# Kernel tuning notes

Measured on AMD Instinct MI355X. Metric: run time of the kernel, lower is better.

## Reference

```python
import jax, jax.numpy as jnp
import numpy as np

N, E = 50000, 800000
IN_DIM, HID, H1, H2, NCLS = 512, 64, 4, 1, 40
NEG_SLOPE = 0.2


def gat_conv(x, src, dst, W, att_src, att_dst, b, heads, ch):
    # x: [N, F_in]; W: [F_in, heads*ch]; att_*: [heads, ch]; b: [heads*ch]
    n = x.shape[0]
    h = (x @ W).reshape(n, heads, ch)                      # [N,H,C]
    a_s = jnp.einsum('nhc,hc->nh', h, att_src)             # [N,H]
    a_d = jnp.einsum('nhc,hc->nh', h, att_dst)             # [N,H]
    e = jax.nn.leaky_relu(a_s[src] + a_d[dst], NEG_SLOPE)  # [E,H]
    # segment softmax over incoming edges of each destination node
    m = jax.ops.segment_max(e, dst, num_segments=n)        # [N,H]
    ex = jnp.exp(e - m[dst])
    s = jax.ops.segment_sum(ex, dst, num_segments=n)       # [N,H]
    alpha = ex / (s[dst] + 1e-16)                          # [E,H]
    out = jax.ops.segment_sum(alpha[:, :, None] * h[src], dst, num_segments=n)
    return out.reshape(n, heads * ch) + b


def setup_inputs() -> dict:
    key = jax.random.key(0)
    ks = jax.random.split(key, 10)
    glorot = lambda k, shp: jax.random.normal(k, shp, jnp.float32) * jnp.sqrt(2.0 / (shp[0] + shp[-1]))
    return {
        'x': jax.random.normal(ks[0], (N, IN_DIM), jnp.float32),
        'edge_index': jax.random.randint(ks[1], (2, E), 0, N, jnp.int64),
        'W1': glorot(ks[2], (IN_DIM, H1 * HID)),
        'att_src1': glorot(ks[3], (H1, HID)),
        'att_dst1': glorot(ks[4], (H1, HID)),
        'b1': jnp.zeros((H1 * HID,), jnp.float32),
        'W2': glorot(ks[5], (H1 * HID, H2 * NCLS)),
        'att_src2': glorot(ks[6], (H2, NCLS)),
        'att_dst2': glorot(ks[7], (H2, NCLS)),
        'b2': jnp.zeros((H2 * NCLS,), jnp.float32),
    }


def reference(x, edge_index, W1, att_src1, att_dst1, b1, W2, att_src2, att_dst2, b2):
    n = x.shape[0]
    loops = jnp.arange(n, dtype=edge_index.dtype)
    src = jnp.concatenate([edge_index[0], loops])  # add self loops (PyG default)
    dst = jnp.concatenate([edge_index[1], loops])
    # dropout layers are identity in eval mode
    h = gat_conv(x, src, dst, W1, att_src1, att_dst1, b1, H1, HID)
    h = jax.nn.elu(h)
    out = gat_conv(h, src, dst, W2, att_src2, att_dst2, b2, H2, NCLS)
    return jax.nn.log_softmax(out, axis=1)
```

## Files before the change

### kernel.cpp

```cpp
#include <hip/hip_runtime.h>
#include <math.h>
#include <stdint.h>


typedef short bf16x8 __attribute__((ext_vector_type(8)));
typedef float f32x4  __attribute__((ext_vector_type(4)));

static __device__ __forceinline__ float leaky(float x){ return x > 0.f ? x : 0.2f*x; }
static __device__ __forceinline__ unsigned short f2bf(float f){
  uint32_t u = __float_as_uint(f);
  uint32_t r = u + 0x7fffu + ((u >> 16) & 1u);
  return (unsigned short)(r >> 16);
}
static __device__ __forceinline__ float bf2f(unsigned short u){
  return __uint_as_float(((uint32_t)u) << 16);
}

__global__ void k_cvt_w(const float* __restrict__ W, unsigned short* __restrict__ wt,
                        int* __restrict__ deg, int n){
  int i = blockIdx.x*blockDim.x + threadIdx.x;
  if (i < n) deg[i] = 0;
  if (i >= 256*64) return;
  int col = i & 255, kg = i >> 8;
  int kt = kg >> 2, kq = kg & 3;
  unsigned short* dst = wt + ((size_t)kt*1024 + kq*256 + col)*8;
  bf16x8 p;
  #pragma unroll
  for (int j=0;j<8;j++) p[j] = (short)f2bf(W[(size_t)(kg*8+j)*256 + col]);
  *(bf16x8*)dst = p;
}

__global__ void k_count(const int* __restrict__ ei, int E, int n, int* __restrict__ deg){
  int i = blockIdx.x*blockDim.x + threadIdx.x;
  int tot = E + n;
  if (i >= tot) return;
  int dst = (i < E) ? ei[E + i] : (i - E);
  atomicAdd(&deg[dst], 1);
}

__global__ __launch_bounds__(256) void k_scan_a(const int* __restrict__ deg,
    int* __restrict__ rowstart, int* __restrict__ bsum, int n){
  __shared__ int sm[256];
  int b = blockIdx.x, t = threadIdx.x;
  int i = b*256 + t;
  int v = (i < n) ? deg[i] : 0;
  sm[t] = v;
  __syncthreads();
  for (int off=1; off<256; off<<=1){
    int u = (t >= off) ? sm[t-off] : 0;
    __syncthreads();
    sm[t] += u;
    __syncthreads();
  }
  if (i < n) rowstart[i+1] = sm[t];
  if (t == 255) bsum[b] = sm[255];
}
__global__ __launch_bounds__(256) void k_scan_b(int* __restrict__ bsum, int nb){
  __shared__ int sm[256];
  int t = threadIdx.x;
  int v = (t < nb) ? bsum[t] : 0;
  sm[t] = v;
  __syncthreads();
  for (int off=1; off<256; off<<=1){
    int u = (t >= off) ? sm[t-off] : 0;
    __syncthreads();
    sm[t] += u;
    __syncthreads();
  }
  if (t < nb) bsum[t] = sm[t] - v;
}
__global__ __launch_bounds__(256) void k_scan_c(int* __restrict__ rowstart,
    const int* __restrict__ bsum, int* __restrict__ cur, int n){
  int b = blockIdx.x, t = threadIdx.x;
  int i = b*256 + t;
  if (i < n){ rowstart[i+1] += bsum[b]; cur[i] = 0; }
  if (i == 0) rowstart[0] = 0;
}

__global__ __launch_bounds__(256, 6) void k_gemm1_mfma(const float* __restrict__ X,
                                                    const unsigned short* __restrict__ WT,
                                                    const float* __restrict__ SW,
                                                    const float* __restrict__ DW,
                                                    unsigned short* __restrict__ Cb,
                                                    float* __restrict__ as1,
                                                    float* __restrict__ ad1, int M){
  __shared__ __align__(16) unsigned short lA[2][2048];
  __shared__ __align__(16) unsigned short lB[2][4096];
  const int t = threadIdx.x;
  const int lane = t & 63, w = t >> 6;
  const int wx = w & 1, wy = w >> 1;
  const int row0 = blockIdx.x * 64, col0 = blockIdx.y * 128;

  f32x4 acc[2][4];
  #pragma unroll
  for (int i=0;i<2;i++)
    #pragma unroll
    for (int j=0;j<4;j++)
      #pragma unroll
      for (int r=0;r<4;r++) acc[i][j][r] = 0.f;

  const int rA = w*16 + (lane & 15);
  const int kA = lane >> 4;
  const float* xA = X + (size_t)min(row0 + rA, M-1)*512 + kA*8;
  const int aChunk = kA*64 + rA;

  const int c0 = t, c1 = t + 256;
  const unsigned short* bB0 = WT + ((size_t)(c0>>7)*256 + col0 + (c0&127))*8;
  const unsigned short* bB1 = WT + ((size_t)(c1>>7)*256 + col0 + (c1&127))*8;

  const int fkq = lane >> 4, li = lane & 15;

#define ISSUE_B(NXT, KT) do{ \
  __builtin_amdgcn_global_load_lds((const __attribute__((address_space(1))) void*)(bB0 + (size_t)(KT)*8192), \
      (__attribute__((address_space(3))) void*)&lB[NXT][c0*8], 16, 0, 0); \
  __builtin_amdgcn_global_load_lds((const __attribute__((address_space(1))) void*)(bB1 + (size_t)(KT)*8192), \
      (__attribute__((address_space(3))) void*)&lB[NXT][c1*8], 16, 0, 0); }while(0)

#define CVT_WRITE(NXT, S0,S1) do{ \
  bf16x8 p0; \
  p0[0]=(short)f2bf(S0.x); p0[1]=(short)f2bf(S0.y); p0[2]=(short)f2bf(S0.z); p0[3]=(short)f2bf(S0.w); \
  p0[4]=(short)f2bf(S1.x); p0[5]=(short)f2bf(S1.y); p0[6]=(short)f2bf(S1.z); p0[7]=(short)f2bf(S1.w); \
  *(bf16x8*)&lA[NXT][aChunk*8] = p0; }while(0)

#define STEP(T, CUR) do{ \
  float4 n0, n1; \
  if ((T) < 15){ \
    n0 = *(const float4*)(xA + ((T)+1)*32); \
    n1 = *(const float4*)(xA + ((T)+1)*32 + 4); \
    ISSUE_B((CUR)^1, (T)+1); \
  } \
  bf16x8 af[2], bfr[4]; \
  _Pragma("unroll") \
  for (int i=0;i<2;i++) \
    af[i]  = *(const bf16x8*)&lA[CUR][(fkq*64 + wx*32 + i*16 + li)*8]; \
  _Pragma("unroll") \
  for (int j=0;j<4;j++) \
    bfr[j] = *(const bf16x8*)&lB[CUR][(fkq*128 + wy*64 + j*16 + li)*8]; \
  _Pragma("unroll") \
  for (int i=0;i<2;i++) \
    _Pragma("unroll") \
    for (int j=0;j<4;j++) \
      acc[i][j] = __builtin_amdgcn_mfma_f32_16x16x32_bf16(af[i], bfr[j], acc[i][j], 0, 0, 0); \
  if ((T) < 15){ \
    CVT_WRITE((CUR)^1, n0, n1); \
    __syncthreads(); \
  } \
}while(0)

  {
    float4 a0 = *(const float4*)(xA);
    float4 a1 = *(const float4*)(xA + 4);
    ISSUE_B(0, 0);
    CVT_WRITE(0, a0, a1);
    __syncthreads();
  }

  #pragma unroll
  for (int tt = 0; tt < 8; ++tt){
    STEP(2*tt,   (0));
    STEP(2*tt+1, (1));
  }

#undef STEP
#undef CVT_WRITE
#undef ISSUE_B

  #pragma unroll
  for (int i=0;i<2;i++){
    #pragma unroll
    for (int r=0;r<4;r++){
      int row = row0 + wx*32 + i*16 + fkq*4 + r;
      if (row < M){
        #pragma unroll
        for (int j=0;j<4;j++)
          Cb[(size_t)row*256 + col0 + wy*64 + j*16 + li] = f2bf(acc[i][j][r]);
      }
    }
  }

  const int hw = (int)blockIdx.y*2 + wy;
  float sv[4], dv[4];
  #pragma unroll
  for (int j=0;j<4;j++){
    sv[j] = SW[hw*64 + j*16 + li];
    dv[j] = DW[hw*64 + j*16 + li];
  }
  #pragma unroll
  for (int i=0;i<2;i++){
    #pragma unroll
    for (int r=0;r<4;r++){
      float ps = acc[i][0][r]*sv[0] + acc[i][1][r]*sv[1] + acc[i][2][r]*sv[2] + acc[i][3][r]*sv[3];
      float pd = acc[i][0][r]*dv[0] + acc[i][1][r]*dv[1] + acc[i][2][r]*dv[2] + acc[i][3][r]*dv[3];
      #pragma unroll
      for (int o=1;o<16;o<<=1){ ps += __shfl_xor(ps,o); pd += __shfl_xor(pd,o); }
      int row = row0 + wx*32 + i*16 + fkq*4 + r;
      if (li == 0 && row < M){
        as1[row*4 + hw] = ps;
        ad1[row*4 + hw] = pd;
      }
    }
  }
}

__global__ void k_fill(const int* __restrict__ ei, int E, int n,
                       const int* __restrict__ rowstart, int* __restrict__ cur,
                       int* __restrict__ csr,
                       const float* __restrict__ as1, const float* __restrict__ ad1,
                       float* __restrict__ exbuf){
  int i = blockIdx.x*blockDim.x + threadIdx.x;
  int tot = E + n;
  if (i >= tot) return;
  int src, dst;
  if (i < E){ src = ei[i]; dst = ei[E+i]; } else { src = i - E; dst = src; }
  int pos = atomicAdd(&cur[dst], 1);
  int slot = rowstart[dst] + pos;
  csr[slot] = src;
  float4 a = *(const float4*)(as1 + (size_t)src*4);
  float4 d = *(const float4*)(ad1 + (size_t)dst*4);
  float4 ex;
  ex.x = __expf(fminf(leaky(a.x + d.x), 80.f));
  ex.y = __expf(fminf(leaky(a.y + d.y), 80.f));
  ex.z = __expf(fminf(leaky(a.z + d.z), 80.f));
  ex.w = __expf(fminf(leaky(a.w + d.w), 80.f));
  *(float4*)(exbuf + (size_t)slot*4) = ex;
}

__global__ __launch_bounds__(256) void k_agg1(const unsigned short* __restrict__ h1b,
    const float* __restrict__ exbuf,
    const int* __restrict__ rowstart, const int* __restrict__ csr,
    const float* __restrict__ b1, unsigned short* __restrict__ hactb, int n){
  int lane = threadIdx.x & 63;
  int node = blockIdx.x*4 + (threadIdx.x >> 6);
  if (node >= n) return;
  int lo = __builtin_amdgcn_readfirstlane(rowstart[node]);
  int hi = __builtin_amdgcn_readfirstlane(rowstart[node+1]);
  int h = lane >> 4;
  const float* exb = exbuf + h;
  float ax=0.f, ay=0.f, az=0.f, aw=0.f, psum=0.f;
  int e = lo;
  for (; e + 7 < hi; e += 8){
    int s0 = csr[e],   s1 = csr[e+1], s2 = csr[e+2], s3 = csr[e+3];
    int s4 = csr[e+4], s5 = csr[e+5], s6 = csr[e+6], s7 = csr[e+7];
    float e0 = exb[(size_t)e*4],     e1 = exb[(size_t)(e+1)*4],
          e2 = exb[(size_t)(e+2)*4], e3 = exb[(size_t)(e+3)*4],
          e4 = exb[(size_t)(e+4)*4], e5 = exb[(size_t)(e+5)*4],
          e6 = exb[(size_t)(e+6)*4], e7 = exb[(size_t)(e+7)*4];
    ushort4 u0 = *(const ushort4*)(h1b + (size_t)s0*256 + lane*4);
    ushort4 u1 = *(const ushort4*)(h1b + (size_t)s1*256 + lane*4);
    ushort4 u2 = *(const ushort4*)(h1b + (size_t)s2*256 + lane*4);
    ushort4 u3 = *(const ushort4*)(h1b + (size_t)s3*256 + lane*4);
    ushort4 u4 = *(const ushort4*)(h1b + (size_t)s4*256 + lane*4);
    ushort4 u5 = *(const ushort4*)(h1b + (size_t)s5*256 + lane*4);
    ushort4 u6 = *(const ushort4*)(h1b + (size_t)s6*256 + lane*4);
    ushort4 u7 = *(const ushort4*)(h1b + (size_t)s7*256 + lane*4);
    ax += e0*bf2f(u0.x) + e1*bf2f(u1.x) + e2*bf2f(u2.x) + e3*bf2f(u3.x)
        + e4*bf2f(u4.x) + e5*bf2f(u5.x) + e6*bf2f(u6.x) + e7*bf2f(u7.x);
    ay += e0*bf2f(u0.y) + e1*bf2f(u1.y) + e2*bf2f(u2.y) + e3*bf2f(u3.y)
        + e4*bf2f(u4.y) + e5*bf2f(u5.y) + e6*bf2f(u6.y) + e7*bf2f(u7.y);
    az += e0*bf2f(u0.z) + e1*bf2f(u1.z) + e2*bf2f(u2.z) + e3*bf2f(u3.z)
        + e4*bf2f(u4.z) + e5*bf2f(u5.z) + e6*bf2f(u6.z) + e7*bf2f(u7.z);
    aw += e0*bf2f(u0.w) + e1*bf2f(u1.w) + e2*bf2f(u2.w) + e3*bf2f(u3.w)
        + e4*bf2f(u4.w) + e5*bf2f(u5.w) + e6*bf2f(u6.w) + e7*bf2f(u7.w);
    psum += (e0+e1+e2+e3) + (e4+e5+e6+e7);
  }
  for (; e < hi; ++e){
    int s0 = csr[e];
    float e0 = exb[(size_t)e*4];
    ushort4 u0 = *(const ushort4*)(h1b + (size_t)s0*256 + lane*4);
    ax += e0*bf2f(u0.x); ay += e0*bf2f(u0.y); az += e0*bf2f(u0.z); aw += e0*bf2f(u0.w);
    psum += e0;
  }
  float inv = 1.f/(psum + 1e-16f);
  float4 bv = *(const float4*)(b1 + lane*4);
  float o0 = ax*inv + bv.x, o1 = ay*inv + bv.y, o2 = az*inv + bv.z, o3 = aw*inv + bv.w;
  ushort4 r;
  r.x = f2bf(o0 > 0.f ? o0 : expm1f(o0));
  r.y = f2bf(o1 > 0.f ? o1 : expm1f(o1));
  r.z = f2bf(o2 > 0.f ? o2 : expm1f(o2));
  r.w = f2bf(o3 > 0.f ? o3 : expm1f(o3));
  *(ushort4*)(hactb + (size_t)node*256 + lane*4) = r;
}

__global__ __launch_bounds__(256) void k_gemm2(const unsigned short* __restrict__ A,
    const float* __restrict__ B, const float* __restrict__ sw, const float* __restrict__ dw,
    unsigned short* __restrict__ Cb, float* __restrict__ as2, float* __restrict__ ad2, int M){
  __shared__ float Xl[32][129];
  __shared__ float Wl[128*40];
  __shared__ float Sps[32][8], Spd[32][8];
  int t = threadIdx.x;
  int row0 = blockIdx.x*32;
  int r = t & 31, g = t >> 5;
  float acc[5] = {0,0,0,0,0};
  for (int kt=0; kt<256; kt+=128){
    for (int i=t; i<1280; i+=256)
      *(float4*)&Wl[i*4] = *(const float4*)(B + kt*40 + i*4);
    for (int i=t; i<512; i+=256){
      int rr = i >> 4, k8 = i & 15;
      int grow = row0 + rr; if (grow >= M) grow = M-1;
      uint4 v = *(const uint4*)(A + (size_t)grow*256 + kt + k8*8);
      float* xp = &Xl[rr][k8*8];
      xp[0] = __uint_as_float(v.x << 16); xp[1] = __uint_as_float(v.x & 0xffff0000u);
      xp[2] = __uint_as_float(v.y << 16); xp[3] = __uint_as_float(v.y & 0xffff0000u);
      xp[4] = __uint_as_float(v.z << 16); xp[5] = __uint_as_float(v.z & 0xffff0000u);
      xp[6] = __uint_as_float(v.w << 16); xp[7] = __uint_as_float(v.w & 0xffff0000u);
    }
    __syncthreads();
    #pragma unroll 4
    for (int k=0;k<128;++k){
      float a = Xl[r][k];
      const float* wp = &Wl[k*40 + g*5];
      #pragma unroll
      for (int j=0;j<5;++j) acc[j] += a * wp[j];
    }
    __syncthreads();
  }
  int grow = row0 + r;
  float ps = 0.f, pd = 0.f;
  #pragma unroll
  for (int j=0;j<5;++j){
    ps += acc[j] * sw[g*5+j];
    pd += acc[j] * dw[g*5+j];
  }
  Sps[r][g] = ps; Spd[r][g] = pd;
  if (grow < M){
    #pragma unroll
    for (int j=0;j<5;++j) Cb[(size_t)grow*40 + g*5 + j] = f2bf(acc[j]);
  }
  __syncthreads();
  if (t < 32){
    float a = 0.f, b = 0.f;
    #pragma unroll
    for (int g2=0; g2<8; ++g2){ a += Sps[t][g2]; b += Spd[t][g2]; }
    int rw = row0 + t;
    if (rw < M){ as2[rw] = a; ad2[rw] = b; }
  }
}

__global__ __launch_bounds__(256) void k_pre2(const float* __restrict__ as2,
    const float* __restrict__ ad2, const int* __restrict__ rowstart,
    const int* __restrict__ csr, float* __restrict__ ex2, int n){
  int lane = threadIdx.x & 63;
  int node = blockIdx.x*4 + (threadIdx.x >> 6);
  if (node >= n) return;
  int lo = rowstart[node], hi = rowstart[node+1];
  float adn = ad2[node];
  for (int e = lo + lane; e < hi; e += 64)
    ex2[e] = __expf(fminf(leaky(as2[csr[e]] + adn), 80.f));
}

__global__ __launch_bounds__(256) void k_agg2(const unsigned short* __restrict__ h2b,
    const float* __restrict__ ex2,
    const int* __restrict__ rowstart, const int* __restrict__ csr,
    const float* __restrict__ b2, float* __restrict__ out, int n){
  int lane = threadIdx.x & 63;
  int node = blockIdx.x*4 + (threadIdx.x >> 6);
  if (node >= n) return;
  int lo = __builtin_amdgcn_readfirstlane(rowstart[node]);
  int hi = __builtin_amdgcn_readfirstlane(rowstart[node+1]);
  bool act = lane < 40;
  float acc = 0.f, psum = 0.f;
  int e = lo;
  for (; e + 7 < hi; e += 8){
    int s0 = csr[e],   s1 = csr[e+1], s2 = csr[e+2], s3 = csr[e+3];
    int s4 = csr[e+4], s5 = csr[e+5], s6 = csr[e+6], s7 = csr[e+7];
    float e0 = ex2[e],   e1 = ex2[e+1], e2 = ex2[e+2], e3 = ex2[e+3];
    float e4 = ex2[e+4], e5 = ex2[e+5], e6 = ex2[e+6], e7 = ex2[e+7];
    float h0 = act ? bf2f(h2b[(size_t)s0*40 + lane]) : 0.f;
    float h1 = act ? bf2f(h2b[(size_t)s1*40 + lane]) : 0.f;
    float h2 = act ? bf2f(h2b[(size_t)s2*40 + lane]) : 0.f;
    float h3 = act ? bf2f(h2b[(size_t)s3*40 + lane]) : 0.f;
    float h4 = act ? bf2f(h2b[(size_t)s4*40 + lane]) : 0.f;
    float h5 = act ? bf2f(h2b[(size_t)s5*40 + lane]) : 0.f;
    float h6 = act ? bf2f(h2b[(size_t)s6*40 + lane]) : 0.f;
    float h7 = act ? bf2f(h2b[(size_t)s7*40 + lane]) : 0.f;
    acc += e0*h0 + e1*h1 + e2*h2 + e3*h3 + e4*h4 + e5*h5 + e6*h6 + e7*h7;
    psum += (e0+e1+e2+e3) + (e4+e5+e6+e7);
  }
  for (; e < hi; ++e){
    int s0 = csr[e]; float e0 = ex2[e];
    acc += e0 * (act ? bf2f(h2b[(size_t)s0*40 + lane]) : 0.f);
    psum += e0;
  }
  float ov = acc/(psum + 1e-16f) + (act ? b2[lane] : 0.f);
  float v = act ? ov : -INFINITY;
  float mx = v;
  #pragma unroll
  for (int o=1;o<64;o<<=1) mx = fmaxf(mx, __shfl_xor(mx,o));
  float ev = act ? __expf(ov - mx) : 0.f;
  float se = ev;
  #pragma unroll
  for (int o=1;o<64;o<<=1) se += __shfl_xor(se,o);
  if (act) out[(size_t)node*40 + lane] = (ov - mx) - __logf(se);
}

extern "C" void kernel_launch(void* const* d_in, const int* in_sizes, int n_in,
                              void* d_out, int out_size, void* d_ws, size_t ws_size,
                              hipStream_t stream){
  const float* x   = (const float*)d_in[0];
  const int*   ei  = (const int*)d_in[1];
  const float* W1  = (const float*)d_in[2];
  const float* s1w = (const float*)d_in[3];
  const float* d1w = (const float*)d_in[4];
  const float* b1  = (const float*)d_in[5];
  const float* W2  = (const float*)d_in[6];
  const float* s2w = (const float*)d_in[7];
  const float* d2w = (const float*)d_in[8];
  const float* b2  = (const float*)d_in[9];
  float* out = (float*)d_out;

  const int N  = in_sizes[0] / 512;
  const int E  = in_sizes[1] / 2;
  const int Et = E + N;

  float* f = (float*)d_ws;
  unsigned short* h1b   = (unsigned short*)f;  f += (size_t)N*128;
  unsigned short* hactb = (unsigned short*)f;  f += (size_t)N*128;
  float* as1  = f;  f += (size_t)N*4;
  float* ad1  = f;  f += (size_t)N*4;
  float* as2  = f;  f += N;
  float* ad2  = f;  f += N;
  unsigned short* w1t = (unsigned short*)f;  f += 256*512/2;
  unsigned short* h2b = (unsigned short*)f;  f += (size_t)N*40/2 + 64;
  float* exbuf = f;  f += (size_t)Et*4;
  float* ex2   = f;  f += Et;
  int* ip = (int*)f;
  int* rowstart = ip;  ip += (N + 4) & ~3;
  int* deg      = ip;  ip += N;
  int* cur      = ip;  ip += N;
  int* csr      = ip;  ip += Et;
  int* bsum     = ip;  ip += 256;

  int nb4 = (N + 3) / 4;
  int nbs = (N + 255) / 256;
  k_cvt_w<<<nbs, 256, 0, stream>>>(W1, w1t, deg, N);
  k_count<<<(Et+255)/256, 256, 0, stream>>>(ei, E, N, deg);
  k_scan_a<<<nbs, 256, 0, stream>>>(deg, rowstart, bsum, N);
  k_scan_b<<<1, 256, 0, stream>>>(bsum, nbs);
  k_scan_c<<<nbs, 256, 0, stream>>>(rowstart, bsum, cur, N);
  k_gemm1_mfma<<<dim3((N+63)/64, 2), 256, 0, stream>>>(x, w1t, s1w, d1w, h1b, as1, ad1, N);
  k_fill <<<(Et+255)/256, 256, 0, stream>>>(ei, E, N, rowstart, cur, csr, as1, ad1, exbuf);
  k_agg1 <<<nb4, 256, 0, stream>>>(h1b, exbuf, rowstart, csr, b1, hactb, N);
  k_gemm2<<<(N+31)/32, 256, 0, stream>>>(hactb, W2, s2w, d2w, h2b, as2, ad2, N);
  k_pre2 <<<nb4, 256, 0, stream>>>(as2, ad2, rowstart, csr, ex2, N);
  k_agg2 <<<nb4, 256, 0, stream>>>(h2b, ex2, rowstart, csr, b2, out, N);
}
```

Baseline: 456.9 us.

## Register-prefetch GEMM tiles two steps ahead and relax occupancy bound

Replaces the direct global-to-LDS loads of the weight tile with register loads, and prefetches both A and B tiles two k-steps ahead in two register sets before writing them to the LDS double buffer. A custom barrier waits only on LDS counters, so global loads stay in flight across the barrier. Launch bounds drop from 6 to 4 waves per SIMD to allow the extra registers. The aim is to hide global latency behind the MFMA work, at the cost of higher register pressure and lower occupancy.

Result: no change. 455.3 us (-0.4%).

```diff
diff --git a/kernel.cpp b/kernel.cpp
--- a/kernel.cpp
+++ b/kernel.cpp
@@ -77,7 +77,7 @@
   if (i == 0) rowstart[0] = 0;
 }
 
-__global__ __launch_bounds__(256, 6) void k_gemm1_mfma(const float* __restrict__ X,
+__global__ __launch_bounds__(256, 4) void k_gemm1_mfma(const float* __restrict__ X,
                                                     const unsigned short* __restrict__ WT,
                                                     const float* __restrict__ SW,
                                                     const float* __restrict__ DW,
@@ -110,25 +110,29 @@
 
   const int fkq = lane >> 4, li = lane & 15;
 
-#define ISSUE_B(NXT, KT) do{ \
-  __builtin_amdgcn_global_load_lds((const __attribute__((address_space(1))) void*)(bB0 + (size_t)(KT)*8192), \
-      (__attribute__((address_space(3))) void*)&lB[NXT][c0*8], 16, 0, 0); \
-  __builtin_amdgcn_global_load_lds((const __attribute__((address_space(1))) void*)(bB1 + (size_t)(KT)*8192), \
-      (__attribute__((address_space(3))) void*)&lB[NXT][c1*8], 16, 0, 0); }while(0)
-
-#define CVT_WRITE(NXT, S0,S1) do{ \
+  float4 pA0, pA1, qA0, qA1;
+  uint4  pB0, pB1, qB0, qB1;
+
+#define LOAD_T(A0,A1,B0,B1, T) do{ \
+  A0 = *(const float4*)(xA + (T)*32); \
+  A1 = *(const float4*)(xA + (T)*32 + 4); \
+  B0 = *(const uint4*)(bB0 + (size_t)(T)*8192); \
+  B1 = *(const uint4*)(bB1 + (size_t)(T)*8192); }while(0)
+
+#define WRITE_T(NXT, A0,A1,B0,B1) do{ \
   bf16x8 p0; \
-  p0[0]=(short)f2bf(S0.x); p0[1]=(short)f2bf(S0.y); p0[2]=(short)f2bf(S0.z); p0[3]=(short)f2bf(S0.w); \
-  p0[4]=(short)f2bf(S1.x); p0[5]=(short)f2bf(S1.y); p0[6]=(short)f2bf(S1.z); p0[7]=(short)f2bf(S1.w); \
-  *(bf16x8*)&lA[NXT][aChunk*8] = p0; }while(0)
-
-#define STEP(T, CUR) do{ \
-  float4 n0, n1; \
-  if ((T) < 15){ \
-    n0 = *(const float4*)(xA + ((T)+1)*32); \
-    n1 = *(const float4*)(xA + ((T)+1)*32 + 4); \
-    ISSUE_B((CUR)^1, (T)+1); \
-  } \
+  p0[0]=(short)f2bf(A0.x); p0[1]=(short)f2bf(A0.y); p0[2]=(short)f2bf(A0.z); p0[3]=(short)f2bf(A0.w); \
+  p0[4]=(short)f2bf(A1.x); p0[5]=(short)f2bf(A1.y); p0[6]=(short)f2bf(A1.z); p0[7]=(short)f2bf(A1.w); \
+  *(bf16x8*)&lA[NXT][aChunk*8] = p0; \
+  *(uint4*)&lB[NXT][c0*8] = B0; \
+  *(uint4*)&lB[NXT][c1*8] = B1; }while(0)
+
+#define BARRIER() do{ \
+  asm volatile("s_waitcnt lgkmcnt(0)" ::: "memory"); \
+  __builtin_amdgcn_s_barrier(); \
+  asm volatile("" ::: "memory"); }while(0)
+
+#define STEP(T, CUR, A0,A1,B0,B1) do{ \
   bf16x8 af[2], bfr[4]; \
   _Pragma("unroll") \
   for (int i=0;i<2;i++) \
@@ -142,28 +146,30 @@
     for (int j=0;j<4;j++) \
       acc[i][j] = __builtin_amdgcn_mfma_f32_16x16x32_bf16(af[i], bfr[j], acc[i][j], 0, 0, 0); \
   if ((T) < 15){ \
-    CVT_WRITE((CUR)^1, n0, n1); \
-    __syncthreads(); \
+    WRITE_T((CUR)^1, A0,A1,B0,B1); \
+    if ((T) <= 12) LOAD_T(A0,A1,B0,B1, (T)+3); \
+    BARRIER(); \
   } \
 }while(0)
 
   {
-    float4 a0 = *(const float4*)(xA);
-    float4 a1 = *(const float4*)(xA + 4);
-    ISSUE_B(0, 0);
-    CVT_WRITE(0, a0, a1);
-    __syncthreads();
+    LOAD_T(pA0,pA1,pB0,pB1, 0);
+    WRITE_T(0, pA0,pA1,pB0,pB1);
+    LOAD_T(pA0,pA1,pB0,pB1, 1);
+    LOAD_T(qA0,qA1,qB0,qB1, 2);
+    BARRIER();
   }
 
   #pragma unroll
   for (int tt = 0; tt < 8; ++tt){
-    STEP(2*tt,   (0));
-    STEP(2*tt+1, (1));
+    STEP(2*tt,   (0), pA0,pA1,pB0,pB1);
+    STEP(2*tt+1, (1), qA0,qA1,qB0,qB1);
   }
 
 #undef STEP
-#undef CVT_WRITE
-#undef ISSUE_B
+#undef BARRIER
+#undef WRITE_T
+#undef LOAD_T
 
   #pragma unroll
   for (int i=0;i<2;i++){
```
